# Performance work log

Hardware: AMD Instinct MI355X
Metric: run time of the kernel (lower is better)

The kernel has to match this reference:

```python
import jax, jax.numpy as jnp
import numpy as np

B, NV, NK = 256, 10475, 144
MV, MK = 778, 21
NB, KN = 8192, 9
TOT_ITR, SW = 5, 0.5


def axis_angle_to_matrix(aa):
    # Rodrigues formula, aa: [B,3] -> [B,3,3]
    angle = jnp.linalg.norm(aa, axis=-1, keepdims=True)
    axis = aa / (angle + 1e-8)
    x, y, z = axis[..., 0], axis[..., 1], axis[..., 2]
    c = jnp.cos(angle[..., 0]); s = jnp.sin(angle[..., 0]); C = 1.0 - c
    R = jnp.stack([
        jnp.stack([c + x * x * C, x * y * C - z * s, x * z * C + y * s], -1),
        jnp.stack([y * x * C + z * s, c + y * y * C, y * z * C - x * s], -1),
        jnp.stack([z * x * C - y * s, z * y * C + x * s, c + z * z * C], -1)], -2)
    return R


def rigid_align(X, Y):
    # Umeyama w/o scale (pytorch3d corresponding_points_alignment): X @ R + T ~= Y
    muX = X.mean(1, keepdims=True); muY = Y.mean(1, keepdims=True)
    C = jnp.einsum('bni,bnj->bij', X - muX, Y - muY)
    U, S, Vt = jnp.linalg.svd(C)
    d = jnp.sign(jnp.linalg.det(U) * jnp.linalg.det(Vt))
    e = jnp.stack([jnp.ones_like(d), jnp.ones_like(d), d], -1)
    R = jnp.einsum('bij,bj,bjk->bik', U, e, Vt)
    T = muY[:, 0] - jnp.einsum('bi,bij->bj', muX[:, 0], R)
    return R, T


def combine_smplx_mano(smplx_vert, smplx_kpt, rv, rk, rpose, lv, lk, lpose,
                       rigid_align_idx, r_align_smplx, l_align_smplx,
                       rhand_vertex_idx, lhand_vertex_idx, r_kpt_idx, l_kpt_idx):
    # undo hand root rotation (torch.inverse on rotation matrices)
    Rr = jnp.linalg.inv(axis_angle_to_matrix(rpose))
    rv = jnp.einsum('bij,bnj->bni', Rr, rv); rk = jnp.einsum('bij,bnj->bni', Rr, rk)
    Rl = jnp.linalg.inv(axis_angle_to_matrix(lpose))
    lv = jnp.einsum('bij,bnj->bni', Rl, lv); lk = jnp.einsum('bij,bnj->bni', Rl, lk)
    # rigid alignment of MANO keypoints to SMPL-X hand keypoints
    R, T = rigid_align(rk[:, rigid_align_idx], smplx_kpt[:, r_align_smplx])
    rv = jnp.einsum('bni,bij->bnj', rv, R) + T[:, None]
    rk = jnp.einsum('bni,bij->bnj', rk, R) + T[:, None]
    R, T = rigid_align(lk[:, rigid_align_idx], smplx_kpt[:, l_align_smplx])
    lv = jnp.einsum('bni,bij->bnj', lv, R) + T[:, None]
    lk = jnp.einsum('bni,bij->bnj', lk, R) + T[:, None]
    # scatter MANO verts/kpts into SMPL-X mesh (torch scatter_ -> .at[].set)
    smplx_vert = smplx_vert.at[:, rhand_vertex_idx].set(rv)
    smplx_vert = smplx_vert.at[:, lhand_vertex_idx].set(lv)
    smplx_kpt = smplx_kpt.at[:, r_kpt_idx].set(rk)
    smplx_kpt = smplx_kpt.at[:, l_kpt_idx].set(lk)
    return smplx_vert, smplx_kpt


def smooth_hand_boundary(v, hand_boundary_idx, vert_neighbor_idxs):
    vn = vert_neighbor_idxs[hand_boundary_idx]                     # [NB, KN]
    mask = vn != -1
    safe = jnp.where(mask, vn, 0)
    num_valid = jnp.maximum(mask.sum(-1), 1).astype(v.dtype)        # [NB]
    maskf = mask.astype(v.dtype)[None, :, :, None]
    for _ in range(TOT_ITR):
        npos = v[:, safe] * maskf                                   # [B, NB, KN, 3]
        nmean = npos.sum(2) / num_valid[None, :, None]
        upd = (1.0 - SW) * v[:, hand_boundary_idx] + SW * nmean
        v = v.at[:, hand_boundary_idx].set(upd)
    return v


def setup_inputs():
    key = jax.random.key(0)
    k = jax.random.split(key, 8)
    rng = np.random.default_rng(0)
    vperm = rng.permutation(NV)
    kperm = rng.permutation(NK)
    vn = rng.integers(0, NV, size=(NV, KN))
    vn[rng.random((NV, KN)) < 0.2] = -1  # -1 padding like smpl_x.vert_neighbor_idxs
    return {
        'smplx_vert_cam': jax.random.normal(k[0], (B, NV, 3), jnp.float32),
        'smplx_kpt_cam': jax.random.normal(k[1], (B, NK, 3), jnp.float32),
        'rmano_vert_cam': jax.random.normal(k[2], (B, MV, 3), jnp.float32),
        'rmano_kpt_cam': jax.random.normal(k[3], (B, MK, 3), jnp.float32),
        'rhand_root_pose': jax.random.normal(k[4], (B, 3), jnp.float32),
        'lmano_vert_cam': jax.random.normal(k[5], (B, MV, 3), jnp.float32),
        'lmano_kpt_cam': jax.random.normal(k[6], (B, MK, 3), jnp.float32),
        'lhand_root_pose': jax.random.normal(k[7], (B, 3), jnp.float32),
        'rigid_align_idx': jnp.asarray(rng.permutation(MK), jnp.int32),
        'r_align_smplx': jnp.asarray(kperm[:MK], jnp.int32),
        'l_align_smplx': jnp.asarray(kperm[MK:2 * MK], jnp.int32),
        'rhand_vertex_idx': jnp.asarray(vperm[:MV], jnp.int32),
        'lhand_vertex_idx': jnp.asarray(vperm[MV:2 * MV], jnp.int32),
        'r_kpt_idx': jnp.asarray(kperm[:MK], jnp.int32),
        'l_kpt_idx': jnp.asarray(kperm[MK:2 * MK], jnp.int32),
        'hand_boundary_idx': jnp.asarray(rng.choice(NV, NB, replace=False), jnp.int32),
        'vert_neighbor_idxs': jnp.asarray(vn, jnp.int32),
    }


def reference(smplx_vert_cam, smplx_kpt_cam, rmano_vert_cam, rmano_kpt_cam,
              rhand_root_pose, lmano_vert_cam, lmano_kpt_cam, lhand_root_pose,
              rigid_align_idx, r_align_smplx, l_align_smplx,
              rhand_vertex_idx, lhand_vertex_idx, r_kpt_idx, l_kpt_idx,
              hand_boundary_idx, vert_neighbor_idxs):
    v, _ = combine_smplx_mano(
        smplx_vert_cam, smplx_kpt_cam, rmano_vert_cam, rmano_kpt_cam,
        rhand_root_pose, lmano_vert_cam, lmano_kpt_cam, lhand_root_pose,
        rigid_align_idx, r_align_smplx, l_align_smplx,
        rhand_vertex_idx, lhand_vertex_idx, r_kpt_idx, l_kpt_idx)
    v = smooth_hand_boundary(v, hand_boundary_idx, vert_neighbor_idxs)
    return v
```

## Files before the change

### kernel.cpp

```cpp
#include <hip/hip_runtime.h>

#define BB    256
#define NVERT 10475
#define NKPT  144
#define MVERT 778
#define MKPT  21
#define NBDRY 8192
#define KNB   9
#define ITERS 5
#define NV3   (NVERT * 3)
#define MV3   (MVERT * 3)

typedef float f32x4 __attribute__((ext_vector_type(4)));

static __device__ __forceinline__ float bfu(unsigned hi16) {
    return __uint_as_float(hi16);
}
static __device__ __forceinline__ unsigned f2bf(float f) {
    unsigned u = __float_as_uint(f);
    u += 0x7FFFu + ((u >> 16) & 1u);
    return u >> 16;
}
static __device__ __forceinline__ void pack_one(unsigned short* msh16, unsigned p, float val) {
    unsigned v = p / 3u;
    unsigned c = p - v * 3u;
    msh16[v * 4u + c] = (unsigned short)f2bf(val);
}

static __device__ __forceinline__ float frcp(float x)  { return __builtin_amdgcn_rcpf(x); }
static __device__ __forceinline__ float frsq(float x)  { return __builtin_amdgcn_rsqf(x); }
static __device__ __forceinline__ float fsqrt_(float x){ return __builtin_amdgcn_sqrtf(x); }

static __device__ __forceinline__ void stage_load(const float* __restrict__ g,
                                                  float* sh, int n, int t, int nt) {
    unsigned lead = (4u - ((unsigned)(((size_t)g) >> 2) & 3u)) & 3u;
    unsigned nb4 = ((unsigned)n - lead) >> 2;
    if (t == 0) for (unsigned e = 0; e < lead; ++e) sh[e] = g[e];
    if (t == 1) for (unsigned e = lead + 4u * nb4; e < (unsigned)n; ++e) sh[e] = g[e];
    const f32x4* g4 = (const f32x4*)(g + lead);
    for (unsigned i4 = (unsigned)t; i4 < nb4; i4 += (unsigned)nt) {
        f32x4 q = g4[i4];
        unsigned p = lead + 4u * i4;
        sh[p] = q.x; sh[p + 1] = q.y; sh[p + 2] = q.z; sh[p + 3] = q.w;
    }
}

#define JROT(DP, DQ, EPQ, A1P, A1Q, A2P, A2Q, VP0, VQ0, VP1, VQ1, VP2, VQ2, VP3, VQ3) { \
    float apq = EPQ; \
    float th = (DQ - DP) * 0.5f * frcp(apq); \
    float t = copysignf(frcp(fabsf(th) + fsqrt_(th*th + 1.0f)), th); \
    t = (fabsf(apq) > 1e-30f) ? t : 0.0f; \
    float cj = frsq(t*t + 1.0f); \
    float sj = t * cj; \
    DP -= t * apq; DQ += t * apq; EPQ = 0.0f; \
    { float x_ = A1P, y_ = A1Q; A1P = cj*x_ - sj*y_; A1Q = sj*x_ + cj*y_; } \
    { float x_ = A2P, y_ = A2Q; A2P = cj*x_ - sj*y_; A2Q = sj*x_ + cj*y_; } \
    { float x_ = VP0, y_ = VQ0; VP0 = cj*x_ - sj*y_; VQ0 = sj*x_ + cj*y_; } \
    { float x_ = VP1, y_ = VQ1; VP1 = cj*x_ - sj*y_; VQ1 = sj*x_ + cj*y_; } \
    { float x_ = VP2, y_ = VQ2; VP2 = cj*x_ - sj*y_; VQ2 = sj*x_ + cj*y_; } \
    { float x_ = VP3, y_ = VQ3; VP3 = cj*x_ - sj*y_; VQ3 = sj*x_ + cj*y_; } \
}

#define JSWEEP \
    JROT(D0,D1,E01, E02,E12, E03,E13, V00,V01,V10,V11,V20,V21,V30,V31) \
    JROT(D0,D2,E02, E01,E12, E03,E23, V00,V02,V10,V12,V20,V22,V30,V32) \
    JROT(D0,D3,E03, E01,E13, E02,E23, V00,V03,V10,V13,V20,V23,V30,V33) \
    JROT(D1,D2,E12, E01,E02, E13,E23, V01,V02,V11,V12,V21,V22,V31,V32) \
    JROT(D1,D3,E13, E01,E03, E12,E23, V01,V03,V11,V13,V21,V23,V31,V33) \
    JROT(D2,D3,E23, E02,E03, E12,E13, V02,V03,V12,V13,V22,V23,V32,V33)

static __device__ void compute_align(
    int b, int h,
    const float* __restrict__ skpt, const float* __restrict__ rkpt,
    const float* __restrict__ lkpt, const float* __restrict__ rpose,
    const float* __restrict__ lpose, const int* __restrict__ perm,
    const int* __restrict__ ralign, const int* __restrict__ lalign,
    float* o)
{
    const float* pose = (h ? lpose : rpose) + b * 3;
    const float* kpt  = (h ? lkpt : rkpt) + (size_t)b * MKPT * 3;
    const int* alidx  = h ? lalign : ralign;

    float ax = pose[0], ay = pose[1], az = pose[2];
    float ang = fsqrt_(ax*ax + ay*ay + az*az);
    float ia = frcp(ang + 1e-8f);
    float x = ax*ia, y = ay*ia, z = az*ia;
    float c = __cosf(ang), s = __sinf(ang), Cc = 1.0f - c;
    float A00 = c + x*x*Cc,   A01 = x*y*Cc - z*s, A02 = x*z*Cc + y*s;
    float A10 = y*x*Cc + z*s, A11 = c + y*y*Cc,   A12 = y*z*Cc - x*s;
    float A20 = z*x*Cc - y*s, A21 = z*y*Cc + x*s, A22 = c + z*z*Cc;

    float sX0=0,sX1=0,sX2=0, sY0=0,sY1=0,sY2=0;
    float S00=0,S01=0,S02=0,S10=0,S11=0,S12=0,S20=0,S21=0,S22=0;
    #pragma unroll
    for (int n = 0; n < MKPT; ++n) {
        int pi = perm[n];
        float p0 = kpt[pi*3+0], p1 = kpt[pi*3+1], p2 = kpt[pi*3+2];
        float X0 = A00*p0 + A10*p1 + A20*p2;
        float X1 = A01*p0 + A11*p1 + A21*p2;
        float X2 = A02*p0 + A12*p1 + A22*p2;
        int qi = alidx[n];
        const float* yp = skpt + ((size_t)b * NKPT + qi) * 3;
        float Y0 = yp[0], Y1 = yp[1], Y2 = yp[2];
        sX0 += X0; sX1 += X1; sX2 += X2;
        sY0 += Y0; sY1 += Y1; sY2 += Y2;
        S00 += X0*Y0; S01 += X0*Y1; S02 += X0*Y2;
        S10 += X1*Y0; S11 += X1*Y1; S12 += X1*Y2;
        S20 += X2*Y0; S21 += X2*Y1; S22 += X2*Y2;
    }
    const float invN = 1.0f / (float)MKPT;
    float C00 = S00 - sX0*sY0*invN, C01 = S01 - sX0*sY1*invN, C02 = S02 - sX0*sY2*invN;
    float C10 = S10 - sX1*sY0*invN, C11 = S11 - sX1*sY1*invN, C12 = S12 - sX1*sY2*invN;
    float C20 = S20 - sX2*sY0*invN, C21 = S21 - sX2*sY1*invN, C22 = S22 - sX2*sY2*invN;

    float D0 = C00 + C11 + C22;
    float E01 = C21 - C12, E02 = C02 - C20, E03 = C10 - C01;
    float D1 = C00 - C11 - C22, E12 = C01 + C10, E13 = C02 + C20;
    float D2 = -C00 + C11 - C22, E23 = C12 + C21;
    float D3 = -C00 - C11 + C22;

    float V00=1,V01=0,V02=0,V03=0;
    float V10=0,V11=1,V12=0,V13=0;
    float V20=0,V21=0,V22=1,V23=0;
    float V30=0,V31=0,V32=0,V33=1;

    JSWEEP JSWEEP JSWEEP JSWEEP JSWEEP JSWEEP

    float dm = D0, w = V00, qx = V10, qy = V20, qz = V30;
    bool c1 = D1 > dm; dm = c1?D1:dm; w = c1?V01:w; qx = c1?V11:qx; qy = c1?V21:qy; qz = c1?V31:qz;
    bool c2 = D2 > dm; dm = c2?D2:dm; w = c2?V02:w; qx = c2?V12:qx; qy = c2?V22:qy; qz = c2?V32:qz;
    bool c3 = D3 > dm;                w = c3?V03:w; qx = c3?V13:qx; qy = c3?V23:qy; qz = c3?V33:qz;

    float R00 = 1.0f - 2.0f*(qy*qy + qz*qz), R01 = 2.0f*(qx*qy - w*qz), R02 = 2.0f*(qx*qz + w*qy);
    float R10 = 2.0f*(qx*qy + w*qz), R11 = 1.0f - 2.0f*(qx*qx + qz*qz), R12 = 2.0f*(qy*qz - w*qx);
    float R20 = 2.0f*(qx*qz - w*qy), R21 = 2.0f*(qy*qz + w*qx), R22 = 1.0f - 2.0f*(qx*qx + qy*qy);

    float mX0 = sX0*invN, mX1 = sX1*invN, mX2 = sX2*invN;
    float mY0 = sY0*invN, mY1 = sY1*invN, mY2 = sY2*invN;

    o[0]  = A00*R00 + A01*R10 + A02*R20;
    o[1]  = A00*R01 + A01*R11 + A02*R21;
    o[2]  = A00*R02 + A01*R12 + A02*R22;
    o[3]  = A10*R00 + A11*R10 + A12*R20;
    o[4]  = A10*R01 + A11*R11 + A12*R21;
    o[5]  = A10*R02 + A11*R12 + A12*R22;
    o[6]  = A20*R00 + A21*R10 + A22*R20;
    o[7]  = A20*R01 + A21*R11 + A22*R21;
    o[8]  = A20*R02 + A21*R12 + A22*R22;
    o[9]  = mY0 - (mX0*R00 + mX1*R10 + mX2*R20);
    o[10] = mY1 - (mX0*R01 + mX1*R11 + mX2*R21);
    o[11] = mY2 - (mX0*R02 + mX1*R12 + mX2*R22);
}

__global__ __launch_bounds__(128) void setup_kernel(
    const float* __restrict__ skpt, const float* __restrict__ rkpt,
    const float* __restrict__ lkpt, const float* __restrict__ rpose,
    const float* __restrict__ lpose, const int* __restrict__ perm,
    const int* __restrict__ ralign, const int* __restrict__ lalign,
    const int* __restrict__ bidx, const int* __restrict__ vnbr,
    float* __restrict__ aff, unsigned* __restrict__ tab)
{
    const int g = blockIdx.x;
    if (g < 4) {
        int t = g * 128 + threadIdx.x;
        compute_align(t >> 1, t & 1, skpt, rkpt, lkpt, rpose, lpose,
                      perm, ralign, lalign, aff + t * 12);
        return;
    }
    int j = (g - 4) * 128 + threadIdx.x;
    int bi = bidx[j];
    const int* row = vnbr + (size_t)bi * KNB;
    unsigned n[9]; unsigned cnt = 0;
    #pragma unroll
    for (int e = 0; e < 9; ++e) {
        int vv = row[e];
        if (vv >= 0) { n[e] = (unsigned)vv; ++cnt; }
        else         { n[e] = (unsigned)NVERT; }
    }
    if (cnt == 0) cnt = 1;
    tab[0 * NBDRY + j] = n[0] | (n[1] << 14);
    tab[1 * NBDRY + j] = n[2] | (n[3] << 14);
    tab[2 * NBDRY + j] = n[4] | (n[5] << 14);
    tab[3 * NBDRY + j] = n[6] | (n[7] << 14);
    tab[4 * NBDRY + j] = n[8] | ((unsigned)bi << 14) | (cnt << 28);
}

__global__ __launch_bounds__(1024, 1) void fused_kernel(
    const float* __restrict__ svert,
    const float* __restrict__ rv,
    const float* __restrict__ lv,
    const int*   __restrict__ ridx,
    const int*   __restrict__ lidx,
    const float* __restrict__ aff,
    const unsigned* __restrict__ tab,
    float*       __restrict__ out)
{
    __shared__ __align__(16) unsigned short msh16[(NVERT + 1) * 4];
    __shared__ __align__(16) float hstage[2 * MV3];
    __shared__ float affsh[24];
    const int b = blockIdx.x;
    const int tid = threadIdx.x;

    if (tid == 0) *((uint2*)(msh16 + NVERT * 4)) = make_uint2(0u, 0u);
    if (tid < 24) affsh[tid] = aff[b * 24 + tid];
    {
        const float* g = svert + (size_t)b * NV3;
        unsigned lead = (4u - ((unsigned)(((size_t)g) >> 2) & 3u)) & 3u;
        unsigned nb4 = ((unsigned)NV3 - lead) >> 2;
        if (tid == 0) for (unsigned e = 0; e < lead; ++e) pack_one(msh16, e, g[e]);
        if (tid == 1) for (unsigned e = lead + 4u * nb4; e < (unsigned)NV3; ++e) pack_one(msh16, e, g[e]);
        const f32x4* g4 = (const f32x4*)(g + lead);
        for (unsigned i4 = (unsigned)tid; i4 < nb4; i4 += 1024u) {
            f32x4 q = g4[i4];
            unsigned p = lead + 4u * i4;
            pack_one(msh16, p,     q.x);
            pack_one(msh16, p + 1, q.y);
            pack_one(msh16, p + 2, q.z);
            pack_one(msh16, p + 3, q.w);
        }
        stage_load(rv + (size_t)b * MV3, hstage,       MV3, tid, 1024);
        stage_load(lv + (size_t)b * MV3, hstage + MV3, MV3, tid, 1024);
    }
    unsigned w0[8], w1[8], w2[8], w3[8], w4[8];
    #pragma unroll
    for (int k = 0; k < 8; ++k) {
        int j = k * 1024 + tid;
        w0[k] = tab[j];
        w1[k] = tab[NBDRY + j];
        w2[k] = tab[2 * NBDRY + j];
        w3[k] = tab[3 * NBDRY + j];
        w4[k] = tab[4 * NBDRY + j];
    }
    __syncthreads();

    for (int i = tid; i < 2 * MVERT; i += 1024) {
        int h = (i >= MVERT) ? 1 : 0;
        int nn = i - h * MVERT;
        const int* hidx = h ? lidx : ridx;
        const float* M = affsh + h * 12;
        const float* p = hstage + h * MV3 + nn * 3;
        float p0 = p[0], p1 = p[1], p2 = p[2];
        float o0 = p0 * M[0] + p1 * M[3] + p2 * M[6] + M[9];
        float o1 = p0 * M[1] + p1 * M[4] + p2 * M[7] + M[10];
        float o2 = p0 * M[2] + p1 * M[5] + p2 * M[8] + M[11];
        ((uint2*)msh16)[hidx[nn]] = make_uint2(f2bf(o0) | (f2bf(o1) << 16), f2bf(o2));
    }
    __syncthreads();

    const uint2* mesh = (const uint2*)msh16;

    uint2 up[8];
    #pragma unroll
    for (int k = 0; k < 8; ++k) up[k] = mesh[(w4[k] >> 14) & 0x3FFFu];

#define NB_GATHER(idx) { uint2 m = mesh[(idx)]; \
        sx += bfu(m.x << 16); sy += bfu(m.x & 0xFFFF0000u); sz += bfu(m.y << 16); }
    for (int itr = 0; itr < ITERS; ++itr) {
        #pragma unroll
        for (int k = 0; k < 8; ++k) {
            float sx = 0.f, sy = 0.f, sz = 0.f;
            NB_GATHER(w0[k] & 0x3FFFu);
            NB_GATHER((w0[k] >> 14) & 0x3FFFu);
            NB_GATHER(w1[k] & 0x3FFFu);
            NB_GATHER((w1[k] >> 14) & 0x3FFFu);
            NB_GATHER(w2[k] & 0x3FFFu);
            NB_GATHER((w2[k] >> 14) & 0x3FFFu);
            NB_GATHER(w3[k] & 0x3FFFu);
            NB_GATHER((w3[k] >> 14) & 0x3FFFu);
            NB_GATHER(w4[k] & 0x3FFFu);
            float hinv = 0.5f * frcp((float)(w4[k] >> 28));
            float ux = 0.5f * bfu(up[k].x << 16)         + hinv * sx;
            float uy = 0.5f * bfu(up[k].x & 0xFFFF0000u) + hinv * sy;
            float uz = 0.5f * bfu(up[k].y << 16)         + hinv * sz;
            up[k] = make_uint2(f2bf(ux) | (f2bf(uy) << 16), f2bf(uz));
        }
        __syncthreads();
        #pragma unroll
        for (int k = 0; k < 8; ++k) {
            ((uint2*)msh16)[(w4[k] >> 14) & 0x3FFFu] = up[k];
        }
        __syncthreads();
    }
#undef NB_GATHER

    float* dst = out + (size_t)b * NV3;
    const unsigned lead = (4u - ((unsigned)(((size_t)dst) >> 2) & 3u)) & 3u;
#define COMP(i, val) { unsigned v_ = (i) / 3u; unsigned c_ = (i) - v_ * 3u; \
        uint2 m_ = mesh[v_]; \
        val = (c_ == 0u) ? bfu(m_.x << 16) : (c_ == 1u) ? bfu(m_.x & 0xFFFF0000u) : bfu(m_.y << 16); }
    if ((unsigned)tid < lead) {
        float v; COMP((unsigned)tid, v);
        dst[tid] = v;
    }
    const unsigned nb4 = ((unsigned)NV3 - lead) >> 2;
    f32x4* dst4 = (f32x4*)(dst + lead);
    for (unsigned i4 = (unsigned)tid; i4 < nb4; i4 += 1024u) {
        unsigned i0 = lead + 4u * i4;
        f32x4 o;
        COMP(i0 + 0u, o.x);
        COMP(i0 + 1u, o.y);
        COMP(i0 + 2u, o.z);
        COMP(i0 + 3u, o.w);
        dst4[i4] = o;
    }
    const unsigned done = lead + 4u * nb4;
    if ((unsigned)tid < (unsigned)NV3 - done) {
        float v; COMP(done + (unsigned)tid, v);
        dst[done + tid] = v;
    }
#undef COMP
}

extern "C" void kernel_launch(void* const* d_in, const int* in_sizes, int n_in,
                              void* d_out, int out_size, void* d_ws, size_t ws_size,
                              hipStream_t stream) {
    const float* svert  = (const float*)d_in[0];
    const float* skpt   = (const float*)d_in[1];
    const float* rv     = (const float*)d_in[2];
    const float* rk     = (const float*)d_in[3];
    const float* rpose  = (const float*)d_in[4];
    const float* lv     = (const float*)d_in[5];
    const float* lk     = (const float*)d_in[6];
    const float* lpose  = (const float*)d_in[7];
    const int*   perm   = (const int*)d_in[8];
    const int*   ralign = (const int*)d_in[9];
    const int*   lalign = (const int*)d_in[10];
    const int*   ridx   = (const int*)d_in[11];
    const int*   lidx   = (const int*)d_in[12];
    const int*   bidx   = (const int*)d_in[15];
    const int*   vnbr   = (const int*)d_in[16];
    float* out = (float*)d_out;

    float*    aff = (float*)d_ws;
    unsigned* tab = (unsigned*)((char*)d_ws + 24576);

    setup_kernel<<<68, 128, 0, stream>>>(skpt, rk, lk, rpose, lpose,
                                         perm, ralign, lalign, bidx, vnbr,
                                         aff, tab);
    fused_kernel<<<BB, 1024, 0, stream>>>(svert, rv, lv, ridx, lidx,
                                          aff, tab, out);
}
```

Before: 55.63 us.

## Precompute static neighbor sums and sort boundary rows by dynamic neighbor count

Each boundary vertex's neighbors are split into ones that change during smoothing (they are themselves boundary vertices) and ones that stay fixed. The fixed-neighbor sum is computed once, stored in bf16 in shared memory and reused across all iterations, so each iteration only gathers the changing neighbors. A new single-block sort kernel reorders boundary rows by (dynamic, static) counts so the variable-length loops diverge less within a wavefront. This adds an extra kernel launch and a larger shared-memory footprint. Storing the fixed sum in bf16 adds one more rounding step.

```diff
diff --git a/kernel.cpp b/kernel.cpp
--- a/kernel.cpp
+++ b/kernel.cpp
@@ -158,7 +158,7 @@
     const float* __restrict__ lpose, const int* __restrict__ perm,
     const int* __restrict__ ralign, const int* __restrict__ lalign,
     const int* __restrict__ bidx, const int* __restrict__ vnbr,
-    float* __restrict__ aff, unsigned* __restrict__ tab)
+    float* __restrict__ aff, unsigned* __restrict__ raw)
 {
     const int g = blockIdx.x;
     if (g < 4) {
@@ -167,22 +167,67 @@
                       perm, ralign, lalign, aff + t * 12);
         return;
     }
-    int j = (g - 4) * 128 + threadIdx.x;
+    __shared__ unsigned char flag[NVERT];
+    const int tid = threadIdx.x;
+    for (int i = tid; i < NVERT; i += 128) flag[i] = 0;
+    __syncthreads();
+    for (int j = tid; j < NBDRY; j += 128) flag[bidx[j]] = 1;
+    __syncthreads();
+    int j = (g - 4) * 128 + tid;
     int bi = bidx[j];
     const int* row = vnbr + (size_t)bi * KNB;
-    unsigned n[9]; unsigned cnt = 0;
+    unsigned slot[9];
+    #pragma unroll
+    for (int e = 0; e < 9; ++e) slot[e] = (unsigned)NVERT;
+    unsigned dc = 0, sc = 0;
     #pragma unroll
     for (int e = 0; e < 9; ++e) {
-        int vv = row[e];
-        if (vv >= 0) { n[e] = (unsigned)vv; ++cnt; }
-        else         { n[e] = (unsigned)NVERT; }
-    }
-    if (cnt == 0) cnt = 1;
-    tab[0 * NBDRY + j] = n[0] | (n[1] << 14);
-    tab[1 * NBDRY + j] = n[2] | (n[3] << 14);
-    tab[2 * NBDRY + j] = n[4] | (n[5] << 14);
-    tab[3 * NBDRY + j] = n[6] | (n[7] << 14);
-    tab[4 * NBDRY + j] = n[8] | ((unsigned)bi << 14) | (cnt << 28);
+        int v = row[e];
+        if (v >= 0) {
+            if (flag[v]) slot[dc++] = (unsigned)v;
+            else         slot[8 - (sc++)] = (unsigned)v;
+        }
+    }
+    unsigned vcnt = dc + sc;
+    if (vcnt == 0u) vcnt = 1u;
+    raw[0 * NBDRY + j] = slot[0] | (slot[1] << 14) | (dc << 28);
+    raw[1 * NBDRY + j] = slot[2] | (slot[3] << 14) | (vcnt << 28);
+    raw[2 * NBDRY + j] = slot[4] | (slot[5] << 14);
+    raw[3 * NBDRY + j] = slot[6] | (slot[7] << 14);
+    raw[4 * NBDRY + j] = slot[8] | ((unsigned)bi << 14) | (sc << 28);
+}
+
+__global__ __launch_bounds__(1024) void sort_kernel(
+    const unsigned* __restrict__ raw, unsigned* __restrict__ tab)
+{
+    __shared__ unsigned hist[160];
+    const int tid = threadIdx.x;
+    if (tid < 160) hist[tid] = 0;
+    __syncthreads();
+    unsigned key[8];
+    #pragma unroll
+    for (int k = 0; k < 8; ++k) {
+        int j = k * 1024 + tid;
+        unsigned a0 = raw[j], a4 = raw[4 * NBDRY + j];
+        key[k] = ((a0 >> 28) << 4) | (a4 >> 28);
+        atomicAdd(&hist[key[k]], 1u);
+    }
+    __syncthreads();
+    if (tid == 0) {
+        unsigned acc = 0;
+        for (int i = 0; i < 160; ++i) { unsigned c = hist[i]; hist[i] = acc; acc += c; }
+    }
+    __syncthreads();
+    #pragma unroll
+    for (int k = 0; k < 8; ++k) {
+        int j = k * 1024 + tid;
+        unsigned pos = atomicAdd(&hist[key[k]], 1u);
+        tab[pos]             = raw[j];
+        tab[NBDRY + pos]     = raw[NBDRY + j];
+        tab[2 * NBDRY + pos] = raw[2 * NBDRY + j];
+        tab[3 * NBDRY + pos] = raw[3 * NBDRY + j];
+        tab[4 * NBDRY + pos] = raw[4 * NBDRY + j];
+    }
 }
 
 __global__ __launch_bounds__(1024, 1) void fused_kernel(
@@ -195,13 +240,16 @@
     const unsigned* __restrict__ tab,
     float*       __restrict__ out)
 {
-    __shared__ __align__(16) unsigned short msh16[(NVERT + 1) * 4];
-    __shared__ __align__(16) float hstage[2 * MV3];
+    __shared__ __align__(16) unsigned long long pool64[(83808 + 65536) / 8];
     __shared__ float affsh[24];
+    unsigned short* msh16 = (unsigned short*)pool64;
+    uint2* meshw = (uint2*)pool64;
+    float* hstage = (float*)((char*)pool64 + 83808);
+    uint2* ssum   = (uint2*)((char*)pool64 + 83808);
     const int b = blockIdx.x;
     const int tid = threadIdx.x;
 
-    if (tid == 0) *((uint2*)(msh16 + NVERT * 4)) = make_uint2(0u, 0u);
+    if (tid == 0) meshw[NVERT] = make_uint2(0u, 0u);
     if (tid < 24) affsh[tid] = aff[b * 24 + tid];
     {
         const float* g = svert + (size_t)b * NV3;
@@ -243,32 +291,49 @@
         float o0 = p0 * M[0] + p1 * M[3] + p2 * M[6] + M[9];
         float o1 = p0 * M[1] + p1 * M[4] + p2 * M[7] + M[10];
         float o2 = p0 * M[2] + p1 * M[5] + p2 * M[8] + M[11];
-        ((uint2*)msh16)[hidx[nn]] = make_uint2(f2bf(o0) | (f2bf(o1) << 16), f2bf(o2));
-    }
-    __syncthreads();
-
-    const uint2* mesh = (const uint2*)msh16;
+        meshw[hidx[nn]] = make_uint2(f2bf(o0) | (f2bf(o1) << 16), f2bf(o2));
+    }
+    __syncthreads();
+
+#define ADD3(IDX, X, Y, Z) { uint2 m_ = meshw[(IDX)]; \
+        X += bfu(m_.x << 16); Y += bfu(m_.x & 0xFFFF0000u); Z += bfu(m_.y << 16); }
 
     uint2 up[8];
     #pragma unroll
-    for (int k = 0; k < 8; ++k) up[k] = mesh[(w4[k] >> 14) & 0x3FFFu];
-
-#define NB_GATHER(idx) { uint2 m = mesh[(idx)]; \
-        sx += bfu(m.x << 16); sy += bfu(m.x & 0xFFFF0000u); sz += bfu(m.y << 16); }
+    for (int k = 0; k < 8; ++k) {
+        unsigned a0 = w0[k], a1 = w1[k], a2 = w2[k], a3 = w3[k], a4 = w4[k];
+        up[k] = meshw[(a4 >> 14) & 0x3FFFu];
+        int sc = (int)(a4 >> 28);
+        float tx = 0.f, ty = 0.f, tz = 0.f;
+        if (sc > 0) ADD3(a4 & 0x3FFFu, tx, ty, tz)
+        if (sc > 1) ADD3((a3 >> 14) & 0x3FFFu, tx, ty, tz)
+        if (sc > 2) ADD3(a3 & 0x3FFFu, tx, ty, tz)
+        if (sc > 3) ADD3((a2 >> 14) & 0x3FFFu, tx, ty, tz)
+        if (sc > 4) ADD3(a2 & 0x3FFFu, tx, ty, tz)
+        if (sc > 5) ADD3((a1 >> 14) & 0x3FFFu, tx, ty, tz)
+        if (sc > 6) ADD3(a1 & 0x3FFFu, tx, ty, tz)
+        if (sc > 7) ADD3((a0 >> 14) & 0x3FFFu, tx, ty, tz)
+        if (sc > 8) ADD3(a0 & 0x3FFFu, tx, ty, tz)
+        ssum[k * 1024 + tid] = make_uint2(f2bf(tx) | (f2bf(ty) << 16), f2bf(tz));
+    }
+
     for (int itr = 0; itr < ITERS; ++itr) {
         #pragma unroll
         for (int k = 0; k < 8; ++k) {
-            float sx = 0.f, sy = 0.f, sz = 0.f;
-            NB_GATHER(w0[k] & 0x3FFFu);
-            NB_GATHER((w0[k] >> 14) & 0x3FFFu);
-            NB_GATHER(w1[k] & 0x3FFFu);
-            NB_GATHER((w1[k] >> 14) & 0x3FFFu);
-            NB_GATHER(w2[k] & 0x3FFFu);
-            NB_GATHER((w2[k] >> 14) & 0x3FFFu);
-            NB_GATHER(w3[k] & 0x3FFFu);
-            NB_GATHER((w3[k] >> 14) & 0x3FFFu);
-            NB_GATHER(w4[k] & 0x3FFFu);
-            float hinv = 0.5f * frcp((float)(w4[k] >> 28));
+            unsigned a0 = w0[k], a1 = w1[k], a2 = w2[k], a3 = w3[k], a4 = w4[k];
+            int dc = (int)(a0 >> 28);
+            uint2 sv = ssum[k * 1024 + tid];
+            float sx = bfu(sv.x << 16), sy = bfu(sv.x & 0xFFFF0000u), sz = bfu(sv.y << 16);
+            if (dc > 0) ADD3(a0 & 0x3FFFu, sx, sy, sz)
+            if (dc > 1) ADD3((a0 >> 14) & 0x3FFFu, sx, sy, sz)
+            if (dc > 2) ADD3(a1 & 0x3FFFu, sx, sy, sz)
+            if (dc > 3) ADD3((a1 >> 14) & 0x3FFFu, sx, sy, sz)
+            if (dc > 4) ADD3(a2 & 0x3FFFu, sx, sy, sz)
+            if (dc > 5) ADD3((a2 >> 14) & 0x3FFFu, sx, sy, sz)
+            if (dc > 6) ADD3(a3 & 0x3FFFu, sx, sy, sz)
+            if (dc > 7) ADD3((a3 >> 14) & 0x3FFFu, sx, sy, sz)
+            if (dc > 8) ADD3(a4 & 0x3FFFu, sx, sy, sz)
+            float hinv = 0.5f * frcp((float)((a1 >> 28) & 0xFu));
             float ux = 0.5f * bfu(up[k].x << 16)         + hinv * sx;
             float uy = 0.5f * bfu(up[k].x & 0xFFFF0000u) + hinv * sy;
             float uz = 0.5f * bfu(up[k].y << 16)         + hinv * sz;
@@ -277,12 +342,13 @@
         __syncthreads();
         #pragma unroll
         for (int k = 0; k < 8; ++k) {
-            ((uint2*)msh16)[(w4[k] >> 14) & 0x3FFFu] = up[k];
+            meshw[(w4[k] >> 14) & 0x3FFFu] = up[k];
         }
         __syncthreads();
     }
-#undef NB_GATHER
-
+#undef ADD3
+
+    const uint2* mesh = (const uint2*)msh16;
     float* dst = out + (size_t)b * NV3;
     const unsigned lead = (4u - ((unsigned)(((size_t)dst) >> 2) & 3u)) & 3u;
 #define COMP(i, val) { unsigned v_ = (i) / 3u; unsigned c_ = (i) - v_ * 3u; \
@@ -332,11 +398,13 @@
     float* out = (float*)d_out;
 
     float*    aff = (float*)d_ws;
-    unsigned* tab = (unsigned*)((char*)d_ws + 24576);
+    unsigned* raw = (unsigned*)((char*)d_ws + 24576);
+    unsigned* tab = (unsigned*)((char*)d_ws + 24576 + 163840);
 
     setup_kernel<<<68, 128, 0, stream>>>(skpt, rk, lk, rpose, lpose,
                                          perm, ralign, lalign, bidx, vnbr,
-                                         aff, tab);
+                                         aff, raw);
+    sort_kernel<<<1, 1024, 0, stream>>>(raw, tab);
     fused_kernel<<<BB, 1024, 0, stream>>>(svert, rv, lv, ridx, lidx,
                                           aff, tab, out);
 }
```

Measured after the change: 89.11 us. 1.6x slower.
